# Kernel tuning notes

Hardware: AMD Instinct MI355X
Metric: run time of the kernel (lower is better)

The kernel has to match this reference:

```python
import jax, jax.numpy as jnp
import numpy as np

B, S, H, D = 2, 2048, 16, 64
BLK_Q, BLK_K = 16, 256  # layout row-block = 16 query rows, col-block = 256 key cols


def setup_inputs() -> dict:
    key = jax.random.key(0)
    qkv = jax.random.normal(key, (B, S, 3, H, D), dtype=jnp.float32)
    nq, nk = S // BLK_Q, S // BLK_K  # 128, 8
    layout = np.zeros((nq, nk), dtype=np.int32)
    rows = np.arange(nq)
    layout[rows, (rows * BLK_Q) // BLK_K] = 1  # local diagonal block
    layout[:, 0] = 1                           # global first key block
    return {"qkv": qkv, "layout": jnp.asarray(layout)}


def reference(qkv, layout):
    # qkv: [B, S, 3, H, D], layout: [S//16, S//256] {0,1}
    b, s, _, h, d = qkv.shape
    scale = 1.0 / np.sqrt(d)  # softmax_temp defaults to 1/sqrt(d_keys)
    q = qkv[:, :, 0]  # [B,S,H,D]
    k = qkv[:, :, 1]
    v = qkv[:, :, 2]
    # Expand block layout to a dense [S, S] boolean mask
    mask = jnp.repeat(jnp.repeat(layout.astype(bool), BLK_Q, axis=0), BLK_K, axis=1)[:s, :s]
    scores = jnp.einsum('bshd,bthd->bhst', q, k) * scale  # [B,H,S,S]
    neg_inf = jnp.asarray(-jnp.inf, scores.dtype)
    scores = jnp.where(mask[None, None], scores, neg_inf)
    attn = jax.nn.softmax(scores, axis=-1)  # dropout_p = 0.0 in eval
    out = jnp.einsum('bhst,bthd->bshd', attn, v)  # [B,S,H,D]
    return out
```

## Files before the change

kernel.cpp:

```cpp
#include <hip/hip_runtime.h>

typedef float f32x4 __attribute__((ext_vector_type(4)));
typedef float f32x16 __attribute__((ext_vector_type(16)));
typedef _Float16 f16x8 __attribute__((ext_vector_type(8)));
typedef __fp16 fp16x2 __attribute__((ext_vector_type(2)));
typedef int i32x2 __attribute__((ext_vector_type(2)));

static __device__ __forceinline__ unsigned pk2(float a, float b) {
    fp16x2 r = __builtin_amdgcn_cvt_pkrtz(a, b);
    return __builtin_bit_cast(unsigned, r);
}
static __device__ __forceinline__ f16x8 pk8(float4 a, float4 b) {
    uint4 u; u.x = pk2(a.x, a.y); u.y = pk2(a.z, a.w);
    u.z = pk2(b.x, b.y); u.w = pk2(b.z, b.w);
    return __builtin_bit_cast(f16x8, u);
}

#define MFMA32(A, B, C) __builtin_amdgcn_mfma_f32_32x32x16_f16((A), (B), (C), 0, 0, 0)

__global__ __launch_bounds__(256, 2) void fba_fwd(const float* __restrict__ qkv,
                                                  const int* __restrict__ layout,
                                                  float* __restrict__ out) {
    __shared__ unsigned short Klds[2][64 * 64];
    __shared__ unsigned short Vtlds[2][64 * 64];

    const int bid = blockIdx.x;
    const int vid = (bid & 7) * 64 + (bid >> 3);
    const int b = vid >> 8;
    const int hh = (vid >> 4) & 15;
    const int j = (vid >> 1) & 7;
    const int qh = vid & 1;

    const int tid = threadIdx.x;
    const int w = tid >> 6;
    const int lane = tid & 63;
    const int l31 = lane & 31;
    const int h = lane >> 5;

    const size_t bbase = (size_t)b * 2048 * 3072;
    const int qbase = 256 * j + 128 * qh + 32 * w;

    unsigned kbl = 0; int nact = 0;
    for (int kb = 0; kb < 8; ++kb) {
        int a = 0;
        #pragma unroll
        for (int r = 0; r < 8; ++r) a |= layout[(16 * j + 8 * qh + r) * 8 + kb];
        if (a) { kbl |= (unsigned)kb << (4 * nact); ++nact; }
    }
    kbl = __builtin_amdgcn_readfirstlane(kbl);
    const int ntile = 4 * nact;

    const float SC = 0.18033688f;
    f16x8 qf[4];
    {
        const float* qp = qkv + bbase + (size_t)(qbase + l31) * 3072 + hh * 64;
        #pragma unroll
        for (int ds = 0; ds < 4; ++ds) {
            const float* p0 = qp + ds * 16 + 8 * h;
            float4 x = *(const float4*)p0;
            float4 y = *(const float4*)(p0 + 4);
            float4 xs = {x.x * SC, x.y * SC, x.z * SC, x.w * SC};
            float4 ys = {y.x * SC, y.y * SC, y.z * SC, y.w * SC};
            qf[ds] = pk8(xs, ys);
        }
    }

    f32x16 acc[2];
    acc[0] = (f32x16)(0.f);
    acc[1] = (f32x16)(0.f);
    float lsum = 0.f;

    const int skey = tid >> 4;
    const int sdc  = tid & 15;

    float4 kr0, kr1, kr2, kr3;
    float4 va0, vb0, va1, vb1;

#define STAGE_LOAD(ks_) {                                                           \
    const float* kp_ = qkv + bbase + (size_t)((ks_) + skey) * 3072 + 1024 + hh * 64 + sdc * 4; \
    kr0 = *(const float4*)kp_;                                                      \
    kr1 = *(const float4*)(kp_ + 16 * 3072);                                        \
    kr2 = *(const float4*)(kp_ + 32 * 3072);                                        \
    kr3 = *(const float4*)(kp_ + 48 * 3072);                                        \
    const float* vp_ = qkv + bbase + (size_t)((ks_) + 2 * skey) * 3072 + 2048 + hh * 64 + sdc * 4; \
    va0 = *(const float4*)vp_;               vb0 = *(const float4*)(vp_ +      3072); \
    va1 = *(const float4*)(vp_ + 32 * 3072); vb1 = *(const float4*)(vp_ + 33 * 3072); \
}

#define WK1(m, krm, KB) *(uint2*)((char*)(KB) + ((((skey + 16 * (m)) * 128 + sdc * 8)) ^ ((skey & 7) << 4))) = \
    make_uint2(pk2(krm.x, krm.y), pk2(krm.z, krm.w));
#define WV1(p, vam, vbm, VB) {                                                      \
    const float* A_ = &vam.x; const float* B_ = &vbm.x;                             \
    _Pragma("unroll")                                                               \
    for (int e2 = 0; e2 < 4; ++e2) {                                                \
        int d_ = 4 * sdc + e2;                                                      \
        int off_ = (d_ * 128 + (2 * skey + 32 * (p)) * 2) ^ (((d_ ^ (d_ >> 3)) & 7) << 4); \
        *(unsigned*)((char*)(VB) + off_) = pk2(A_[e2], B_[e2]);                     \
    }                                                                               \
}
#define STAGE_WRITE(nb) {                                                           \
    unsigned short* KB = &Klds[nb][0];                                              \
    WK1(0, kr0, KB) WK1(1, kr1, KB) WK1(2, kr2, KB) WK1(3, kr3, KB)                 \
    unsigned short* VB = &Vtlds[nb][0];                                             \
    WV1(0, va0, vb0, VB) WV1(1, va1, vb1, VB)                                       \
}

#define CHUNK(KB, VB, kt) {                                                         \
    const int key = (kt) * 32 + l31;                                                \
    const int kswz = (l31 & 7) << 4;                                                \
    f16x8 kf[4];                                                                    \
    _Pragma("unroll")                                                               \
    for (int ds = 0; ds < 4; ++ds)                                                  \
        kf[ds] = *(const f16x8*)((const char*)(KB) + ((key * 128 + ds * 32 + h * 16) ^ kswz)); \
    f16x8 vf[2][2];                                                                 \
    _Pragma("unroll")                                                               \
    for (int dt = 0; dt < 2; ++dt) {                                                \
        const int d = dt * 32 + l31;                                                \
        const int vswz = ((d ^ (d >> 3)) & 7) << 4;                                 \
        _Pragma("unroll")                                                           \
        for (int ksi = 0; ksi < 2; ++ksi)                                           \
            vf[dt][ksi] = *(const f16x8*)((const char*)(VB) + ((d * 128 + (kt) * 64 + ksi * 32 + h * 16) ^ vswz)); \
    }                                                                               \
    __builtin_amdgcn_s_setprio(1);                                                  \
    f32x16 st = (f32x16)(0.f);                                                      \
    st = MFMA32(kf[0], qf[0], st);                                                  \
    st = MFMA32(kf[1], qf[1], st);                                                  \
    st = MFMA32(kf[2], qf[2], st);                                                  \
    st = MFMA32(kf[3], qf[3], st);                                                  \
    __builtin_amdgcn_s_setprio(0);                                                  \
    unsigned ulo[4], uhi[4];                                                        \
    float psum = 0.f;                                                               \
    _Pragma("unroll")                                                               \
    for (int jq = 0; jq < 4; ++jq) {                                                \
        float e0 = exp2f(st[4 * jq + 0]), e1 = exp2f(st[4 * jq + 1]);               \
        float e2 = exp2f(st[4 * jq + 2]), e3 = exp2f(st[4 * jq + 3]);               \
        psum += (e0 + e1) + (e2 + e3);                                              \
        ulo[jq] = pk2(e0, e1); uhi[jq] = pk2(e2, e3);                               \
    }                                                                               \
    lsum += psum;                                                                   \
    __builtin_amdgcn_s_setprio(1);                                                  \
    _Pragma("unroll")                                                               \
    for (int ksi = 0; ksi < 2; ++ksi) {                                             \
        i32x2 r0 = __builtin_amdgcn_permlane32_swap((int)ulo[2 * ksi], (int)ulo[2 * ksi + 1], false, false); \
        i32x2 r1 = __builtin_amdgcn_permlane32_swap((int)uhi[2 * ksi], (int)uhi[2 * ksi + 1], false, false); \
        uint4 uw;                                                                   \
        uw.x = (unsigned)r0[0]; uw.y = (unsigned)r1[0];                             \
        uw.z = (unsigned)r0[1]; uw.w = (unsigned)r1[1];                             \
        f16x8 pf = __builtin_bit_cast(f16x8, uw);                                   \
        acc[0] = MFMA32(vf[0][ksi], pf, acc[0]);                                    \
        acc[1] = MFMA32(vf[1][ksi], pf, acc[1]);                                    \
    }                                                                               \
    __builtin_amdgcn_s_setprio(0);                                                  \
}

#define TB(t_) ((int)(((kbl >> (((t_) >> 2) * 4)) & 15) * 256 + ((t_) & 3) * 64))

    STAGE_LOAD(TB(0));
    STAGE_WRITE(0);
    __syncthreads();

    const int ws = w & 1;
    for (int t = 0; t < ntile; ++t) {
        const bool more = (t + 1 < ntile);
        if (more) STAGE_LOAD(TB(t + 1));
        const unsigned short* KB = &Klds[t & 1][0];
        const unsigned short* VB = &Vtlds[t & 1][0];
        CHUNK(KB, VB, (0 ^ ws));
        CHUNK(KB, VB, (1 ^ ws));
        if (more) STAGE_WRITE((t + 1) & 1);
        __syncthreads();
    }

    lsum += __shfl_xor(lsum, 32);
    const float inv = 1.0f / lsum;
    float* op = out + (((size_t)b * 2048 + (qbase + l31)) * 16 + hh) * 64;
    #pragma unroll
    for (int dt = 0; dt < 2; ++dt)
        #pragma unroll
        for (int jq = 0; jq < 4; ++jq) {
            float4 o;
            o.x = acc[dt][4 * jq + 0] * inv;
            o.y = acc[dt][4 * jq + 1] * inv;
            o.z = acc[dt][4 * jq + 2] * inv;
            o.w = acc[dt][4 * jq + 3] * inv;
            *(float4*)(op + dt * 32 + 8 * jq + 4 * h) = o;
        }
}

extern "C" void kernel_launch(void* const* d_in, const int* in_sizes, int n_in,
                              void* d_out, int out_size, void* d_ws, size_t ws_size,
                              hipStream_t stream) {
    const float* qkv = (const float*)d_in[0];
    const int* layout = (const int*)d_in[1];
    float* out = (float*)d_out;
    fba_fwd<<<dim3(512), dim3(256), 0, stream>>>(qkv, layout, out);
}
```

Before: 26.95 us.

## Double tile size to 128 keys per barrier with split two-phase staging

Each LDS buffer now holds 128 keys instead of 64, which halves the number of __syncthreads barriers per key block. The global loads for the next tile are split into two 64-key halves, interleaved with four compute chunks. Each wave starts the chunk rotation at a different offset. This doubles LDS use per block, which may limit occupancy (launch bounds still request 2 blocks per CU), and register pressure stays similar.

```diff
diff --git a/kernel.cpp b/kernel.cpp
--- a/kernel.cpp
+++ b/kernel.cpp
@@ -21,8 +21,8 @@
 __global__ __launch_bounds__(256, 2) void fba_fwd(const float* __restrict__ qkv,
                                                   const int* __restrict__ layout,
                                                   float* __restrict__ out) {
-    __shared__ unsigned short Klds[2][64 * 64];
-    __shared__ unsigned short Vtlds[2][64 * 64];
+    __shared__ unsigned short Klds[2][128 * 64];
+    __shared__ unsigned short Vtlds[2][64 * 128];
 
     const int bid = blockIdx.x;
     const int vid = (bid & 7) * 64 + (bid >> 3);
@@ -48,7 +48,7 @@
         if (a) { kbl |= (unsigned)kb << (4 * nact); ++nact; }
     }
     kbl = __builtin_amdgcn_readfirstlane(kbl);
-    const int ntile = 4 * nact;
+    const int ntile = 2 * nact;
 
     const float SC = 0.18033688f;
     f16x8 qf[4];
@@ -76,7 +76,7 @@
     float4 kr0, kr1, kr2, kr3;
     float4 va0, vb0, va1, vb1;
 
-#define STAGE_LOAD(ks_) {                                                           \
+#define STAGE_LOAD(ks_) {            \
     const float* kp_ = qkv + bbase + (size_t)((ks_) + skey) * 3072 + 1024 + hh * 64 + sdc * 4; \
     kr0 = *(const float4*)kp_;                                                      \
     kr1 = *(const float4*)(kp_ + 16 * 3072);                                        \
@@ -87,22 +87,23 @@
     va1 = *(const float4*)(vp_ + 32 * 3072); vb1 = *(const float4*)(vp_ + 33 * 3072); \
 }
 
-#define WK1(m, krm, KB) *(uint2*)((char*)(KB) + ((((skey + 16 * (m)) * 128 + sdc * 8)) ^ ((skey & 7) << 4))) = \
-    make_uint2(pk2(krm.x, krm.y), pk2(krm.z, krm.w));
-#define WV1(p, vam, vbm, VB) {                                                      \
+#define WK1(m, krm, KB, koff) { int row_ = (koff) + skey + 16 * (m);                \
+    *(uint2*)((char*)(KB) + ((row_ * 128 + sdc * 8) ^ ((skey & 7) << 4))) =         \
+        make_uint2(pk2(krm.x, krm.y), pk2(krm.z, krm.w)); }
+#define WV1(p, vam, vbm, VB, koff) {                                                \
     const float* A_ = &vam.x; const float* B_ = &vbm.x;                             \
     _Pragma("unroll")                                                               \
     for (int e2 = 0; e2 < 4; ++e2) {                                                \
         int d_ = 4 * sdc + e2;                                                      \
-        int off_ = (d_ * 128 + (2 * skey + 32 * (p)) * 2) ^ (((d_ ^ (d_ >> 3)) & 7) << 4); \
+        int off_ = (d_ * 256 + ((koff) + 2 * skey + 32 * (p)) * 2) ^ (((d_ ^ (d_ >> 3)) & 7) << 4); \
         *(unsigned*)((char*)(VB) + off_) = pk2(A_[e2], B_[e2]);                     \
     }                                                                               \
 }
-#define STAGE_WRITE(nb) {                                                           \
+#define STAGE_WRITE(nb, koff) {                                                     \
     unsigned short* KB = &Klds[nb][0];                                              \
-    WK1(0, kr0, KB) WK1(1, kr1, KB) WK1(2, kr2, KB) WK1(3, kr3, KB)                 \
+    WK1(0, kr0, KB, koff) WK1(1, kr1, KB, koff) WK1(2, kr2, KB, koff) WK1(3, kr3, KB, koff) \
     unsigned short* VB = &Vtlds[nb][0];                                             \
-    WV1(0, va0, vb0, VB) WV1(1, va1, vb1, VB)                                       \
+    WV1(0, va0, vb0, VB, koff) WV1(1, va1, vb1, VB, koff)                           \
 }
 
 #define CHUNK(KB, VB, kt) {                                                         \
@@ -119,7 +120,7 @@
         const int vswz = ((d ^ (d >> 3)) & 7) << 4;                                 \
         _Pragma("unroll")                                                           \
         for (int ksi = 0; ksi < 2; ++ksi)                                           \
-            vf[dt][ksi] = *(const f16x8*)((const char*)(VB) + ((d * 128 + (kt) * 64 + ksi * 32 + h * 16) ^ vswz)); \
+            vf[dt][ksi] = *(const f16x8*)((const char*)(VB) + ((d * 256 + (kt) * 64 + ksi * 32 + h * 16) ^ vswz)); \
     }                                                                               \
     __builtin_amdgcn_s_setprio(1);                                                  \
     f32x16 st = (f32x16)(0.f);                                                      \
@@ -153,21 +154,29 @@
     __builtin_amdgcn_s_setprio(0);                                                  \
 }
 
-#define TB(t_) ((int)(((kbl >> (((t_) >> 2) * 4)) & 15) * 256 + ((t_) & 3) * 64))
+#define TB(t_) ((int)(((kbl >> (((t_) >> 1) * 4)) & 15) * 256 + ((t_) & 1) * 128))
 
     STAGE_LOAD(TB(0));
-    STAGE_WRITE(0);
+    STAGE_WRITE(0, 0);
+    STAGE_LOAD(TB(0) + 64);
+    STAGE_WRITE(0, 64);
     __syncthreads();
 
-    const int ws = w & 1;
     for (int t = 0; t < ntile; ++t) {
         const bool more = (t + 1 < ntile);
+        const int cur = t & 1, nxt = (t + 1) & 1;
+        const unsigned short* KB = &Klds[cur][0];
+        const unsigned short* VB = &Vtlds[cur][0];
         if (more) STAGE_LOAD(TB(t + 1));
-        const unsigned short* KB = &Klds[t & 1][0];
-        const unsigned short* VB = &Vtlds[t & 1][0];
-        CHUNK(KB, VB, (0 ^ ws));
-        CHUNK(KB, VB, (1 ^ ws));
-        if (more) STAGE_WRITE((t + 1) & 1);
+        CHUNK(KB, VB, ((0 + w) & 3));
+        CHUNK(KB, VB, ((1 + w) & 3));
+        if (more) {
+            STAGE_WRITE(nxt, 0);
+            STAGE_LOAD(TB(t + 1) + 64);
+        }
+        CHUNK(KB, VB, ((2 + w) & 3));
+        CHUNK(KB, VB, ((3 + w) & 3));
+        if (more) STAGE_WRITE(nxt, 64);
         __syncthreads();
     }
 
```

Result: no change. 27.07 us (+0.4%).

## Merge query halves into 512-thread blocks sharing K/V staging

Applied to the files above, without the earlier changes.

Each block now covers all 256 query rows of a row-block with 8 waves instead of 128 rows with 4 waves, halving the grid to 256 blocks. K/V tiles staged into LDS are reused by twice as many waves, and each thread loads half as much K/V data per stage. The trade-offs are fewer blocks (256 on a GPU with many CUs, which may underfill the device) and larger blocks that are harder to co-schedule. The layout scan now ORs 16 rows per key block.

```diff
diff --git a/kernel.cpp b/kernel.cpp
--- a/kernel.cpp
+++ b/kernel.cpp
@@ -18,18 +18,17 @@
 
 #define MFMA32(A, B, C) __builtin_amdgcn_mfma_f32_32x32x16_f16((A), (B), (C), 0, 0, 0)
 
-__global__ __launch_bounds__(256, 2) void fba_fwd(const float* __restrict__ qkv,
+__global__ __launch_bounds__(512, 2) void fba_fwd(const float* __restrict__ qkv,
                                                   const int* __restrict__ layout,
                                                   float* __restrict__ out) {
     __shared__ unsigned short Klds[2][64 * 64];
     __shared__ unsigned short Vtlds[2][64 * 64];
 
     const int bid = blockIdx.x;
-    const int vid = (bid & 7) * 64 + (bid >> 3);
-    const int b = vid >> 8;
-    const int hh = (vid >> 4) & 15;
-    const int j = (vid >> 1) & 7;
-    const int qh = vid & 1;
+    const int vid = (bid & 7) * 32 + (bid >> 3);
+    const int b = vid >> 7;
+    const int hh = (vid >> 3) & 15;
+    const int j = vid & 7;
 
     const int tid = threadIdx.x;
     const int w = tid >> 6;
@@ -38,13 +37,13 @@
     const int h = lane >> 5;
 
     const size_t bbase = (size_t)b * 2048 * 3072;
-    const int qbase = 256 * j + 128 * qh + 32 * w;
+    const int qbase = 256 * j + 32 * w;
 
     unsigned kbl = 0; int nact = 0;
     for (int kb = 0; kb < 8; ++kb) {
         int a = 0;
         #pragma unroll
-        for (int r = 0; r < 8; ++r) a |= layout[(16 * j + 8 * qh + r) * 8 + kb];
+        for (int r = 0; r < 16; ++r) a |= layout[(16 * j + r) * 8 + kb];
         if (a) { kbl |= (unsigned)kb << (4 * nact); ++nact; }
     }
     kbl = __builtin_amdgcn_readfirstlane(kbl);
@@ -70,39 +69,36 @@
     acc[1] = (f32x16)(0.f);
     float lsum = 0.f;
 
-    const int skey = tid >> 4;
+    const int sk32 = tid >> 4;
     const int sdc  = tid & 15;
 
-    float4 kr0, kr1, kr2, kr3;
-    float4 va0, vb0, va1, vb1;
+    float4 kr0, kr1;
+    float4 va0, vb0;
 
 #define STAGE_LOAD(ks_) {                                                           \
-    const float* kp_ = qkv + bbase + (size_t)((ks_) + skey) * 3072 + 1024 + hh * 64 + sdc * 4; \
+    const float* kp_ = qkv + bbase + (size_t)((ks_) + sk32) * 3072 + 1024 + hh * 64 + sdc * 4; \
     kr0 = *(const float4*)kp_;                                                      \
-    kr1 = *(const float4*)(kp_ + 16 * 3072);                                        \
-    kr2 = *(const float4*)(kp_ + 32 * 3072);                                        \
-    kr3 = *(const float4*)(kp_ + 48 * 3072);                                        \
-    const float* vp_ = qkv + bbase + (size_t)((ks_) + 2 * skey) * 3072 + 2048 + hh * 64 + sdc * 4; \
-    va0 = *(const float4*)vp_;               vb0 = *(const float4*)(vp_ +      3072); \
-    va1 = *(const float4*)(vp_ + 32 * 3072); vb1 = *(const float4*)(vp_ + 33 * 3072); \
+    kr1 = *(const float4*)(kp_ + 32 * 3072);                                        \
+    const float* vp_ = qkv + bbase + (size_t)((ks_) + 2 * sk32) * 3072 + 2048 + hh * 64 + sdc * 4; \
+    va0 = *(const float4*)vp_;                                                      \
+    vb0 = *(const float4*)(vp_ + 3072);                                             \
 }
 
-#define WK1(m, krm, KB) *(uint2*)((char*)(KB) + ((((skey + 16 * (m)) * 128 + sdc * 8)) ^ ((skey & 7) << 4))) = \
-    make_uint2(pk2(krm.x, krm.y), pk2(krm.z, krm.w));
-#define WV1(p, vam, vbm, VB) {                                                      \
-    const float* A_ = &vam.x; const float* B_ = &vbm.x;                             \
+#define STAGE_WRITE(nb) {                                                           \
+    unsigned short* KB = &Klds[nb][0];                                              \
+    const int kswz_ = (sk32 & 7) << 4;                                              \
+    *(uint2*)((char*)KB + (((sk32     ) * 128 + sdc * 8) ^ kswz_)) =                \
+        make_uint2(pk2(kr0.x, kr0.y), pk2(kr0.z, kr0.w));                           \
+    *(uint2*)((char*)KB + (((sk32 + 32) * 128 + sdc * 8) ^ kswz_)) =                \
+        make_uint2(pk2(kr1.x, kr1.y), pk2(kr1.z, kr1.w));                           \
+    unsigned short* VB = &Vtlds[nb][0];                                             \
+    const float* A_ = &va0.x; const float* B_ = &vb0.x;                             \
     _Pragma("unroll")                                                               \
     for (int e2 = 0; e2 < 4; ++e2) {                                                \
         int d_ = 4 * sdc + e2;                                                      \
-        int off_ = (d_ * 128 + (2 * skey + 32 * (p)) * 2) ^ (((d_ ^ (d_ >> 3)) & 7) << 4); \
-        *(unsigned*)((char*)(VB) + off_) = pk2(A_[e2], B_[e2]);                     \
+        int off_ = (d_ * 128 + (2 * sk32) * 2) ^ (((d_ ^ (d_ >> 3)) & 7) << 4);     \
+        *(unsigned*)((char*)VB + off_) = pk2(A_[e2], B_[e2]);                       \
     }                                                                               \
-}
-#define STAGE_WRITE(nb) {                                                           \
-    unsigned short* KB = &Klds[nb][0];                                              \
-    WK1(0, kr0, KB) WK1(1, kr1, KB) WK1(2, kr2, KB) WK1(3, kr3, KB)                 \
-    unsigned short* VB = &Vtlds[nb][0];                                             \
-    WV1(0, va0, vb0, VB) WV1(1, va1, vb1, VB)                                       \
 }
 
 #define CHUNK(KB, VB, kt) {                                                         \
@@ -193,5 +189,5 @@
     const float* qkv = (const float*)d_in[0];
     const int* layout = (const int*)d_in[1];
     float* out = (float*)d_out;
-    fba_fwd<<<dim3(512), dim3(256), 0, stream>>>(qkv, layout, out);
+    fba_fwd<<<dim3(256), dim3(512), 0, stream>>>(qkv, layout, out);
 }
```

New measurement: 28.78 us. 6.8% more time.
